# Performance work log

Measured on AMD Instinct MI355X. Metric: run time of the kernel, lower is better.

Reference implementation:

```python
import jax, jax.numpy as jnp
import numpy as np

B, N, D, WIN = 2, 4096, 256, 16


def setup_inputs() -> dict:
    key = jax.random.key(0)
    ks = jax.random.split(key, 10)
    def lin(k, o, i):
        return 0.02 * jax.random.normal(k, (o, i), jnp.float32)
    W = N // WIN
    return {
        "x": 0.5 * jax.random.normal(ks[0], (B, N, D), jnp.float32),
        "embed_qk": jax.random.normal(ks[1], (3, B, W, WIN, WIN, 3), jnp.float32),
        "act_proj_w": lin(ks[2], D, D), "act_proj_b": jnp.zeros((D,), jnp.float32),
        "proj_ln_g": jnp.ones((D,), jnp.float32), "proj_ln_b": jnp.zeros((D,), jnp.float32),
        "conv_w": lin(ks[3], D, D), "conv_b": jnp.zeros((D,), jnp.float32),
        "q_w": lin(ks[4], D, D), "q_b": jnp.zeros((D,), jnp.float32),
        "k_w": lin(ks[5], D, D), "k_b": jnp.zeros((D,), jnp.float32),
        "p_w": lin(ks[6], 1, 3), "p_b": jnp.zeros((1,), jnp.float32),
        "lin_w": lin(ks[7], D, D), "lin_b": jnp.zeros((D,), jnp.float32),
        "norm_g": jnp.ones((D,), jnp.float32), "norm_b": jnp.zeros((D,), jnp.float32),
    }


def _ln(x, g, b, eps=1e-5):
    m = x.mean(-1, keepdims=True)
    v = ((x - m) ** 2).mean(-1, keepdims=True)
    return (x - m) * jax.lax.rsqrt(v + eps) * g + b


def reference(x, embed_qk, act_proj_w, act_proj_b, proj_ln_g, proj_ln_b,
              conv_w, conv_b, q_w, q_b, k_w, k_b, p_w, p_b,
              lin_w, lin_b, norm_g, norm_b):
    # MSMAttentionLayer: gated residual path
    act_res = jax.nn.silu(x @ act_proj_w.T + act_proj_b)          # (B,N,C)
    h = _ln(x, proj_ln_g, proj_ln_b)
    h = jax.nn.silu(h @ conv_w.T + conv_b)                        # 1x1 conv == per-token linear

    # MSMLMultiHeadAttention, stage=1 (window 4x4=16); N % 16 == 0 so add_row_num = 0
    q = jax.nn.elu(h @ q_w.T + q_b) + 1.0
    k = jax.nn.elu(h @ k_w.T + k_b) + 1.0
    v = h
    Bn, Nn, C = h.shape
    Wn = Nn // WIN
    q_win = q.reshape(Bn, Wn, WIN, C)
    k_win = k.reshape(Bn, Wn, WIN, C)
    v_win = v.reshape(Bn, Wn, WIN, C)
    # learned relative-position bias: Linear(3,1) on embed_qk[stage]
    p = (embed_qk[1] @ p_w.T + p_b)[..., 0]
    # second elu+1 feature map (applied on top of q/k which are already elu+1)
    phi_q = jax.nn.elu(q_win) + 1.0
    phi_k = jax.nn.elu(k_win) + 1.0
    # linear-attention style KV aggregation: reduces over windows w
    KV = jnp.einsum('bwmc,bwmd->bmcd', phi_k, v_win)
    att = jnp.einsum('bwnc,bmcd->bwnmd', phi_q, KV) + p[..., None]
    attn_out = att.reshape(Bn, -1, C)[:, :Nn, :]                  # (B,N,C)

    hid = (attn_out * act_res) @ lin_w.T + lin_b
    return _ln(hid + h, norm_g, norm_b)
```

## Files before the change

kernel.cpp:

```cpp
#include <hip/hip_runtime.h>


#define DIM 256
#define NTOK 4096

typedef __attribute__((ext_vector_type(8))) short short8;
typedef __attribute__((ext_vector_type(4))) short short4v;
typedef __attribute__((ext_vector_type(4))) float f32x4;

__device__ __forceinline__ float silu_f(float z) { return z / (1.f + __expf(-z)); }
__device__ __forceinline__ float elu2_f(float z) { return z > 0.f ? z + 2.f : __expf(z) + 1.f; }

__device__ __forceinline__ short f2bf(float f) {
    union { float f; unsigned u; } v; v.f = f;
    unsigned r = v.u + 0x7fffu + ((v.u >> 16) & 1u);
    return (short)(r >> 16);
}
__device__ __forceinline__ float bf2f(short s) {
    union { unsigned u; float f; } v; v.u = ((unsigned)(unsigned short)s) << 16;
    return v.f;
}
__device__ __forceinline__ short8 cvt8(const float* src) {
    const float4 a = *(const float4*)src;
    const float4 c = *(const float4*)(src + 4);
    short8 s;
    s[0] = f2bf(a.x); s[1] = f2bf(a.y); s[2] = f2bf(a.z); s[3] = f2bf(a.w);
    s[4] = f2bf(c.x); s[5] = f2bf(c.y); s[6] = f2bf(c.z); s[7] = f2bf(c.w);
    return s;
}

__global__ __launch_bounds__(256) void fused_dual(
        const float* __restrict__ XF,
        const float* __restrict__ W0f, const float* __restrict__ b0, short* __restrict__ Y0,
        const float* __restrict__ W1f, const float* __restrict__ b1, short* __restrict__ Y1,
        const float* __restrict__ G, const float* __restrict__ Bt) {
    __shared__ __align__(16) short Xs[64 * 72];
    __shared__ __align__(16) short Ws[64 * 72];
    __shared__ float stats[64][2];
    const int zz = blockIdx.z;
    const float* Wf = zz ? W1f : W0f;
    const float* bias = zz ? b1 : b0;
    short* Y = zz ? Y1 : Y0;
    const int tid = threadIdx.x;
    const int wv = tid >> 6, l = tid & 63;
    const int lr = l & 15, lk = l >> 4;
    const int r0 = blockIdx.x * 64, c0 = blockIdx.y * 64;
    const int wm = (wv >> 1) * 32, wn = (wv & 1) * 32;
    const int sr = tid >> 3, sc = (tid & 7) * 8;

    if (zz) {
        const int prow = tid >> 2, pseg = tid & 3;
        const float* src = XF + (size_t)(r0 + prow) * DIM + pseg * 64;
        float a1 = 0.f, a2 = 0.f;
        #pragma unroll
        for (int j = 0; j < 16; ++j) {
            const float4 v = *(const float4*)(src + j * 4);
            a1 += v.x + v.y + v.z + v.w;
            a2 += v.x * v.x + v.y * v.y + v.z * v.z + v.w * v.w;
        }
        a1 += __shfl_xor(a1, 1); a2 += __shfl_xor(a2, 1);
        a1 += __shfl_xor(a1, 2); a2 += __shfl_xor(a2, 2);
        if (pseg == 0) {
            const float mm = a1 * (1.f / DIM);
            stats[prow][0] = mm;
            stats[prow][1] = rsqrtf(a2 * (1.f / DIM) - mm * mm + 1e-5f);
        }
        __syncthreads();
    }

    f32x4 acc[2][2];
    #pragma unroll
    for (int i = 0; i < 2; ++i)
        #pragma unroll
        for (int j = 0; j < 2; ++j) acc[i][j] = (f32x4){0.f, 0.f, 0.f, 0.f};
    for (int kt = 0; kt < DIM; kt += 64) {
        #pragma unroll
        for (int p = 0; p < 2; ++p) {
            const int row = sr + p * 32;
            const float* src = XF + (size_t)(r0 + row) * DIM + kt + sc;
            const float4 a = *(const float4*)src;
            const float4 c = *(const float4*)(src + 4);
            float v[8] = {a.x, a.y, a.z, a.w, c.x, c.y, c.z, c.w};
            short8 s;
            if (zz) {
                const float mm = stats[row][0], rs = stats[row][1];
                const float4 g1 = *(const float4*)(G + kt + sc);
                const float4 g2 = *(const float4*)(G + kt + sc + 4);
                const float4 t1 = *(const float4*)(Bt + kt + sc);
                const float4 t2 = *(const float4*)(Bt + kt + sc + 4);
                const float gv[8] = {g1.x, g1.y, g1.z, g1.w, g2.x, g2.y, g2.z, g2.w};
                const float bv[8] = {t1.x, t1.y, t1.z, t1.w, t2.x, t2.y, t2.z, t2.w};
                #pragma unroll
                for (int j = 0; j < 8; ++j) s[j] = f2bf((v[j] - mm) * rs * gv[j] + bv[j]);
            } else {
                #pragma unroll
                for (int j = 0; j < 8; ++j) s[j] = f2bf(v[j]);
            }
            *(short8*)&Xs[row * 72 + sc] = s;
        }
        #pragma unroll
        for (int p = 0; p < 2; ++p) {
            const int row = sr + p * 32;
            *(short8*)&Ws[row * 72 + sc] = cvt8(Wf + (size_t)(c0 + row) * DIM + kt + sc);
        }
        __syncthreads();
        #pragma unroll
        for (int kc = 0; kc < 2; ++kc) {
            short8 af[2], bfr[2];
            #pragma unroll
            for (int mi = 0; mi < 2; ++mi)
                af[mi] = *(const short8*)&Xs[(wm + mi * 16 + lr) * 72 + kc * 32 + lk * 8];
            #pragma unroll
            for (int ni = 0; ni < 2; ++ni)
                bfr[ni] = *(const short8*)&Ws[(wn + ni * 16 + lr) * 72 + kc * 32 + lk * 8];
            #pragma unroll
            for (int mi = 0; mi < 2; ++mi)
                #pragma unroll
                for (int ni = 0; ni < 2; ++ni)
                    acc[mi][ni] = __builtin_amdgcn_mfma_f32_16x16x32_bf16(af[mi], bfr[ni], acc[mi][ni], 0, 0, 0);
        }
        __syncthreads();
    }
    #pragma unroll
    for (int mi = 0; mi < 2; ++mi)
        #pragma unroll
        for (int ni = 0; ni < 2; ++ni) {
            const int c = c0 + wn + ni * 16 + lr;
            const float bv = bias[c];
            #pragma unroll
            for (int i = 0; i < 4; ++i) {
                const int r = r0 + wm + mi * 16 + lk * 4 + i;
                Y[(size_t)r * DIM + c] = f2bf(silu_f(acc[mi][ni][i] + bv));
            }
        }
}

__global__ __launch_bounds__(256) void gemm_kq(
        const short* __restrict__ H, const float* __restrict__ Wkf, const float* __restrict__ bk, short* __restrict__ PK,
        const float* __restrict__ Wqf, const float* __restrict__ bq, short* __restrict__ PQ) {
    __shared__ __align__(16) short Xs[64 * 72];
    __shared__ __align__(16) short Ws[64 * 72];
    const int bx = blockIdx.x;
    const bool isq = bx >= 128;
    const float* Wf = isq ? Wqf : Wkf;
    const float* bias = isq ? bq : bk;
    short* Y = isq ? PQ : PK;
    const int r0 = (isq ? bx - 128 : bx) * 64;
    const int c0 = blockIdx.y * 64;
    const int tid = threadIdx.x;
    const int wv = tid >> 6, l = tid & 63;
    const int lr = l & 15, lk = l >> 4;
    const int wm = (wv >> 1) * 32, wn = (wv & 1) * 32;
    const int sr = tid >> 3, sc = (tid & 7) * 8;
    f32x4 acc[2][2];
    #pragma unroll
    for (int i = 0; i < 2; ++i)
        #pragma unroll
        for (int j = 0; j < 2; ++j) acc[i][j] = (f32x4){0.f, 0.f, 0.f, 0.f};
    for (int kt = 0; kt < DIM; kt += 64) {
        #pragma unroll
        for (int p = 0; p < 2; ++p) {
            const int row = sr + p * 32;
            int grow = r0 + row;
            if (isq) grow = ((grow >> 8) << 12) + (grow & 255);
            *(short8*)&Xs[row * 72 + sc] = *(const short8*)(H + (size_t)grow * DIM + kt + sc);
        }
        #pragma unroll
        for (int p = 0; p < 2; ++p) {
            const int row = sr + p * 32;
            *(short8*)&Ws[row * 72 + sc] = cvt8(Wf + (size_t)(c0 + row) * DIM + kt + sc);
        }
        __syncthreads();
        #pragma unroll
        for (int kc = 0; kc < 2; ++kc) {
            short8 af[2], bfr[2];
            #pragma unroll
            for (int mi = 0; mi < 2; ++mi)
                af[mi] = *(const short8*)&Xs[(wm + mi * 16 + lr) * 72 + kc * 32 + lk * 8];
            #pragma unroll
            for (int ni = 0; ni < 2; ++ni)
                bfr[ni] = *(const short8*)&Ws[(wn + ni * 16 + lr) * 72 + kc * 32 + lk * 8];
            #pragma unroll
            for (int mi = 0; mi < 2; ++mi)
                #pragma unroll
                for (int ni = 0; ni < 2; ++ni)
                    acc[mi][ni] = __builtin_amdgcn_mfma_f32_16x16x32_bf16(af[mi], bfr[ni], acc[mi][ni], 0, 0, 0);
        }
        __syncthreads();
    }
    #pragma unroll
    for (int mi = 0; mi < 2; ++mi)
        #pragma unroll
        for (int ni = 0; ni < 2; ++ni) {
            const int c = c0 + wn + ni * 16 + lr;
            const float bv = bias[c];
            #pragma unroll
            for (int i = 0; i < 4; ++i) {
                const int r = r0 + wm + mi * 16 + lk * 4 + i;
                Y[(size_t)r * DIM + c] = f2bf(elu2_f(acc[mi][ni][i] + bv));
            }
        }
}

__global__ __launch_bounds__(256) void kv_mfma(const short* __restrict__ HB, const short* __restrict__ PK,
                                               short* __restrict__ KVT) {
    __shared__ __align__(16) short Hs[64 * 68];
    __shared__ __align__(16) short Ps[64 * 68];
    const int tid = threadIdx.x;
    const int bm = blockIdx.x, b = bm >> 4, m = bm & 15;
    const int d0 = blockIdx.y * 64, c0 = blockIdx.z * 64;
    const int wv = tid >> 6, l = tid & 63;
    const int lr = l & 15, lk = l >> 4;
    const int wd = (wv >> 1) * 32, wc = (wv & 1) * 32;
    f32x4 acc[2][2];
    #pragma unroll
    for (int i = 0; i < 2; ++i)
        #pragma unroll
        for (int j = 0; j < 2; ++j) acc[i][j] = (f32x4){0.f, 0.f, 0.f, 0.f};
    const size_t hbase = (size_t)b * NTOK * DIM;
    const int sr = tid >> 3, sc = (tid & 7) * 8;
    for (int kt = 0; kt < 256; kt += 64) {
        #pragma unroll
        for (int p = 0; p < 2; ++p) {
            const int w = sr + p * 32;
            const size_t gg = hbase + (size_t)((kt + w) * 16 + m) * DIM;
            short8 hv = *(const short8*)(HB + gg + d0 + sc);
            short8 pv = *(const short8*)(PK + gg + c0 + sc);
            *(short4v*)&Hs[w * 68 + sc]     = __builtin_shufflevector(hv, hv, 0, 1, 2, 3);
            *(short4v*)&Hs[w * 68 + sc + 4] = __builtin_shufflevector(hv, hv, 4, 5, 6, 7);
            *(short4v*)&Ps[w * 68 + sc]     = __builtin_shufflevector(pv, pv, 0, 1, 2, 3);
            *(short4v*)&Ps[w * 68 + sc + 4] = __builtin_shufflevector(pv, pv, 4, 5, 6, 7);
        }
        __syncthreads();
        #pragma unroll
        for (int kc = 0; kc < 2; ++kc) {
            const int kb = kc * 32 + lk * 8;
            short8 af[2], bfr[2];
            #pragma unroll
            for (int di = 0; di < 2; ++di)
                #pragma unroll
                for (int i = 0; i < 8; ++i)
                    af[di][i] = Hs[(kb + i) * 68 + wd + di * 16 + lr];
            #pragma unroll
            for (int ci = 0; ci < 2; ++ci)
                #pragma unroll
                for (int i = 0; i < 8; ++i)
                    bfr[ci][i] = Ps[(kb + i) * 68 + wc + ci * 16 + lr];
            #pragma unroll
            for (int di = 0; di < 2; ++di)
                #pragma unroll
                for (int ci = 0; ci < 2; ++ci)
                    acc[di][ci] = __builtin_amdgcn_mfma_f32_16x16x32_bf16(af[di], bfr[ci], acc[di][ci], 0, 0, 0);
        }
        __syncthreads();
    }
    #pragma unroll
    for (int di = 0; di < 2; ++di)
        #pragma unroll
        for (int ci = 0; ci < 2; ++ci)
            #pragma unroll
            for (int i = 0; i < 4; ++i) {
                const int d = d0 + wd + di * 16 + lk * 4 + i;
                const int c = c0 + wc + ci * 16 + lr;
                KVT[((size_t)bm * DIM + d) * DIM + c] = f2bf(acc[di][ci][i]);
            }
}

__global__ __launch_bounds__(256) void attlin(
        const short* __restrict__ PQ, const short* __restrict__ KVT,
        const float* __restrict__ emb, const float* __restrict__ pw, const float* __restrict__ pb,
        const short* __restrict__ AR,
        const float* __restrict__ WLf, const float* __restrict__ bl,
        const short* __restrict__ HB, const float* __restrict__ G, const float* __restrict__ Bt,
        float* __restrict__ Y) {
    __shared__ __align__(16) short Qs[32 * 264];
    __shared__ __align__(16) short AGs[32 * 264];
    __shared__ __align__(16) short Bs[256 * 72];
    __shared__ float s1buf[32][2];
    __shared__ float s2buf[32][2];
    const int tid = threadIdx.x;
    const int wv = tid >> 6, l = tid & 63;
    const int lr = l & 15, lk = l >> 4;
    const int bm = blockIdx.x, b = bm >> 4, m = bm & 15;
    const int q0 = blockIdx.y * 32;
    const int wq = (wv >> 1) * 16;
    const int wd = (wv & 1) * 32;
    const int sr = tid >> 3, sc = (tid & 7) * 8;

    #pragma unroll
    for (int p = 0; p < 4; ++p) {
        const int chunk = tid + p * 256;
        const int row = chunk >> 5, cc = (chunk & 31) * 8;
        *(short8*)&Qs[row * 264 + cc] = *(const short8*)(PQ + (size_t)(b * 256 + q0 + row) * DIM + cc);
    }

    f32x4 accA[4][2];
    #pragma unroll
    for (int i = 0; i < 4; ++i)
        #pragma unroll
        for (int j = 0; j < 2; ++j) accA[i][j] = (f32x4){0.f, 0.f, 0.f, 0.f};
    for (int kt = 0; kt < DIM; kt += 64) {
        #pragma unroll
        for (int p = 0; p < 8; ++p) {
            const int row = sr + p * 32;
            *(short8*)&Bs[row * 72 + sc] = *(const short8*)(KVT + ((size_t)bm * DIM + row) * DIM + kt + sc);
        }
        __syncthreads();
        #pragma unroll
        for (int kc = 0; kc < 2; ++kc) {
            const short8 af = *(const short8*)&Qs[(wq + lr) * 264 + kt + kc * 32 + lk * 8];
            #pragma unroll
            for (int dc = 0; dc < 4; ++dc)
                #pragma unroll
                for (int ni = 0; ni < 2; ++ni) {
                    const short8 bfr = *(const short8*)&Bs[(dc * 64 + wd + ni * 16 + lr) * 72 + kc * 32 + lk * 8];
                    accA[dc][ni] = __builtin_amdgcn_mfma_f32_16x16x32_bf16(af, bfr, accA[dc][ni], 0, 0, 0);
                }
        }
        __syncthreads();
    }
    {
        const float pw0 = pw[0], pw1 = pw[1], pw2 = pw[2], pbv = pb[0];
        #pragma unroll
        for (int i = 0; i < 4; ++i) {
            const int rloc = wq + lk * 4 + i;
            const int qr = q0 + rloc;
            const int widx = qr >> 4, nidx = qr & 15;
            const float* e = emb + ((((size_t)(2 + b) * 256 + widx) * 16 + nidx) * 16 + m) * 3;
            const float pv = e[0] * pw0 + e[1] * pw1 + e[2] * pw2 + pbv;
            const int t = qr * 16 + m;
            #pragma unroll
            for (int dc = 0; dc < 4; ++dc)
                #pragma unroll
                for (int ni = 0; ni < 2; ++ni) {
                    const int d = dc * 64 + wd + ni * 16 + lr;
                    const size_t o = ((size_t)b * NTOK + t) * DIM + d;
                    AGs[rloc * 264 + d] = f2bf((accA[dc][ni][i] + pv) * bf2f(AR[o]));
                }
        }
    }
    __syncthreads();

    const int wn2 = (wv & 1) * 128;
    f32x4 accB[8];
    #pragma unroll
    for (int i = 0; i < 8; ++i) accB[i] = (f32x4){0.f, 0.f, 0.f, 0.f};
    for (int kt = 0; kt < DIM; kt += 64) {
        #pragma unroll
        for (int p = 0; p < 8; ++p) {
            const int row = sr + p * 32;
            *(short8*)&Bs[row * 72 + sc] = cvt8(WLf + (size_t)row * DIM + kt + sc);
        }
        __syncthreads();
        #pragma unroll
        for (int kc = 0; kc < 2; ++kc) {
            const short8 af = *(const short8*)&AGs[(wq + lr) * 264 + kt + kc * 32 + lk * 8];
            #pragma unroll
            for (int ni = 0; ni < 8; ++ni) {
                const short8 bfr = *(const short8*)&Bs[(wn2 + ni * 16 + lr) * 72 + kc * 32 + lk * 8];
                accB[ni] = __builtin_amdgcn_mfma_f32_16x16x32_bf16(af, bfr, accB[ni], 0, 0, 0);
            }
        }
        __syncthreads();
    }
    float s1[4] = {0.f, 0.f, 0.f, 0.f}, s2[4] = {0.f, 0.f, 0.f, 0.f};
    #pragma unroll
    for (int ni = 0; ni < 8; ++ni) {
        const int col = wn2 + ni * 16 + lr;
        const float bv = bl[col];
        #pragma unroll
        for (int i = 0; i < 4; ++i) {
            const int rloc = wq + lk * 4 + i;
            const int t = (q0 + rloc) * 16 + m;
            const float z = accB[ni][i] + bv + bf2f(HB[((size_t)b * NTOK + t) * DIM + col]);
            accB[ni][i] = z;
            s1[i] += z; s2[i] += z * z;
        }
    }
    #pragma unroll
    for (int o = 1; o < 16; o <<= 1) {
        #pragma unroll
        for (int i = 0; i < 4; ++i) {
            s1[i] += __shfl_xor(s1[i], o);
            s2[i] += __shfl_xor(s2[i], o);
        }
    }
    if (lr == 0) {
        #pragma unroll
        for (int i = 0; i < 4; ++i) {
            const int rloc = wq + lk * 4 + i;
            s1buf[rloc][wv & 1] = s1[i];
            s2buf[rloc][wv & 1] = s2[i];
        }
    }
    __syncthreads();
    float mean[4], rstd[4];
    #pragma unroll
    for (int i = 0; i < 4; ++i) {
        const int rloc = wq + lk * 4 + i;
        const float t1 = s1buf[rloc][0] + s1buf[rloc][1];
        const float t2 = s2buf[rloc][0] + s2buf[rloc][1];
        const float mm = t1 * (1.f / DIM);
        mean[i] = mm;
        rstd[i] = rsqrtf(t2 * (1.f / DIM) - mm * mm + 1e-5f);
    }
    #pragma unroll
    for (int ni = 0; ni < 8; ++ni) {
        const int col = wn2 + ni * 16 + lr;
        const float gv = G[col], bv2 = Bt[col];
        #pragma unroll
        for (int i = 0; i < 4; ++i) {
            const int rloc = wq + lk * 4 + i;
            const int t = (q0 + rloc) * 16 + m;
            Y[((size_t)b * NTOK + t) * DIM + col] = (accB[ni][i] - mean[i]) * rstd[i] * gv + bv2;
        }
    }
}

extern "C" void kernel_launch(void* const* d_in, const int* in_sizes, int n_in,
                              void* d_out, int out_size, void* d_ws, size_t ws_size,
                              hipStream_t stream) {
    const float* x   = (const float*)d_in[0];
    const float* emb = (const float*)d_in[1];
    const float* Wa  = (const float*)d_in[2];
    const float* ba  = (const float*)d_in[3];
    const float* lng = (const float*)d_in[4];
    const float* lnb = (const float*)d_in[5];
    const float* Wc  = (const float*)d_in[6];
    const float* bc  = (const float*)d_in[7];
    const float* Wq  = (const float*)d_in[8];
    const float* bq  = (const float*)d_in[9];
    const float* Wk  = (const float*)d_in[10];
    const float* bk  = (const float*)d_in[11];
    const float* pw  = (const float*)d_in[12];
    const float* pb  = (const float*)d_in[13];
    const float* Wl  = (const float*)d_in[14];
    const float* bl  = (const float*)d_in[15];
    const float* ng  = (const float*)d_in[16];
    const float* nb  = (const float*)d_in[17];

    char* ws = (char*)d_ws;
    const size_t MB = 1024 * 1024;
    short* h_bf   = (short*)(ws + 0 * MB);
    short* phik   = (short*)(ws + 4 * MB);
    short* phiq   = (short*)(ws + 8 * MB);
    short* kvT    = (short*)(ws + 9 * MB);
    short* act_bf = (short*)(ws + 13 * MB);

    fused_dual<<<dim3(128, 4, 2), dim3(256), 0, stream>>>(x, Wa, ba, act_bf,
                                                          Wc, bc, h_bf, lng, lnb);
    gemm_kq<<<dim3(136, 4), dim3(256), 0, stream>>>(h_bf, Wk, bk, phik, Wq, bq, phiq);
    kv_mfma<<<dim3(32, 4, 4), dim3(256), 0, stream>>>(h_bf, phik, kvT);
    attlin<<<dim3(32, 8), dim3(256), 0, stream>>>(phiq, kvT, emb, pw, pb, act_bf, Wl, bl,
                                                  h_bf, ng, nb, (float*)d_out);
}
```

Measured before the change: 59.14 us.

## Keep weight slab resident in LDS and loop over multiple row tiles

Both projection GEMM kernels now load a full 64x256 bf16 weight slab into shared memory once per block and reuse it across several 64-row tiles, instead of reconverting fp32 weights every k-step for each tile. Grids shrink (64x4x2 and 66x4), with each block handling 2 row tiles, or 4 for the Q path. This removes redundant global weight loads and fp32-to-bf16 conversion, at the cost of larger LDS use (about 33KB per block) and fewer blocks, which may reduce occupancy and parallelism on a many-CU GPU.

```diff
diff --git a/kernel.cpp b/kernel.cpp
--- a/kernel.cpp
+++ b/kernel.cpp
@@ -29,177 +29,195 @@
     return s;
 }
 
-__global__ __launch_bounds__(256) void fused_dual(
+__global__ __launch_bounds__(256) void gemm_wres_a(
         const float* __restrict__ XF,
-        const float* __restrict__ W0f, const float* __restrict__ b0, short* __restrict__ Y0,
-        const float* __restrict__ W1f, const float* __restrict__ b1, short* __restrict__ Y1,
+        const float* __restrict__ Waf, const float* __restrict__ ba, short* __restrict__ ACT,
+        const float* __restrict__ Wcf, const float* __restrict__ bc, short* __restrict__ H,
         const float* __restrict__ G, const float* __restrict__ Bt) {
+    __shared__ __align__(16) short Wres[64 * 264];
     __shared__ __align__(16) short Xs[64 * 72];
-    __shared__ __align__(16) short Ws[64 * 72];
     __shared__ float stats[64][2];
     const int zz = blockIdx.z;
-    const float* Wf = zz ? W1f : W0f;
-    const float* bias = zz ? b1 : b0;
-    short* Y = zz ? Y1 : Y0;
-    const int tid = threadIdx.x;
-    const int wv = tid >> 6, l = tid & 63;
-    const int lr = l & 15, lk = l >> 4;
-    const int r0 = blockIdx.x * 64, c0 = blockIdx.y * 64;
-    const int wm = (wv >> 1) * 32, wn = (wv & 1) * 32;
-    const int sr = tid >> 3, sc = (tid & 7) * 8;
-
-    if (zz) {
-        const int prow = tid >> 2, pseg = tid & 3;
-        const float* src = XF + (size_t)(r0 + prow) * DIM + pseg * 64;
-        float a1 = 0.f, a2 = 0.f;
-        #pragma unroll
-        for (int j = 0; j < 16; ++j) {
-            const float4 v = *(const float4*)(src + j * 4);
-            a1 += v.x + v.y + v.z + v.w;
-            a2 += v.x * v.x + v.y * v.y + v.z * v.z + v.w * v.w;
-        }
-        a1 += __shfl_xor(a1, 1); a2 += __shfl_xor(a2, 1);
-        a1 += __shfl_xor(a1, 2); a2 += __shfl_xor(a2, 2);
-        if (pseg == 0) {
-            const float mm = a1 * (1.f / DIM);
-            stats[prow][0] = mm;
-            stats[prow][1] = rsqrtf(a2 * (1.f / DIM) - mm * mm + 1e-5f);
-        }
-        __syncthreads();
-    }
-
-    f32x4 acc[2][2];
-    #pragma unroll
-    for (int i = 0; i < 2; ++i)
-        #pragma unroll
-        for (int j = 0; j < 2; ++j) acc[i][j] = (f32x4){0.f, 0.f, 0.f, 0.f};
-    for (int kt = 0; kt < DIM; kt += 64) {
-        #pragma unroll
-        for (int p = 0; p < 2; ++p) {
-            const int row = sr + p * 32;
-            const float* src = XF + (size_t)(r0 + row) * DIM + kt + sc;
-            const float4 a = *(const float4*)src;
-            const float4 c = *(const float4*)(src + 4);
-            float v[8] = {a.x, a.y, a.z, a.w, c.x, c.y, c.z, c.w};
-            short8 s;
-            if (zz) {
-                const float mm = stats[row][0], rs = stats[row][1];
-                const float4 g1 = *(const float4*)(G + kt + sc);
-                const float4 g2 = *(const float4*)(G + kt + sc + 4);
-                const float4 t1 = *(const float4*)(Bt + kt + sc);
-                const float4 t2 = *(const float4*)(Bt + kt + sc + 4);
-                const float gv[8] = {g1.x, g1.y, g1.z, g1.w, g2.x, g2.y, g2.z, g2.w};
-                const float bv[8] = {t1.x, t1.y, t1.z, t1.w, t2.x, t2.y, t2.z, t2.w};
-                #pragma unroll
-                for (int j = 0; j < 8; ++j) s[j] = f2bf((v[j] - mm) * rs * gv[j] + bv[j]);
-            } else {
-                #pragma unroll
-                for (int j = 0; j < 8; ++j) s[j] = f2bf(v[j]);
-            }
-            *(short8*)&Xs[row * 72 + sc] = s;
-        }
-        #pragma unroll
-        for (int p = 0; p < 2; ++p) {
-            const int row = sr + p * 32;
-            *(short8*)&Ws[row * 72 + sc] = cvt8(Wf + (size_t)(c0 + row) * DIM + kt + sc);
-        }
-        __syncthreads();
-        #pragma unroll
-        for (int kc = 0; kc < 2; ++kc) {
-            short8 af[2], bfr[2];
-            #pragma unroll
-            for (int mi = 0; mi < 2; ++mi)
-                af[mi] = *(const short8*)&Xs[(wm + mi * 16 + lr) * 72 + kc * 32 + lk * 8];
-            #pragma unroll
-            for (int ni = 0; ni < 2; ++ni)
-                bfr[ni] = *(const short8*)&Ws[(wn + ni * 16 + lr) * 72 + kc * 32 + lk * 8];
-            #pragma unroll
-            for (int mi = 0; mi < 2; ++mi)
-                #pragma unroll
-                for (int ni = 0; ni < 2; ++ni)
-                    acc[mi][ni] = __builtin_amdgcn_mfma_f32_16x16x32_bf16(af[mi], bfr[ni], acc[mi][ni], 0, 0, 0);
-        }
-        __syncthreads();
-    }
-    #pragma unroll
-    for (int mi = 0; mi < 2; ++mi)
-        #pragma unroll
-        for (int ni = 0; ni < 2; ++ni) {
-            const int c = c0 + wn + ni * 16 + lr;
-            const float bv = bias[c];
-            #pragma unroll
-            for (int i = 0; i < 4; ++i) {
-                const int r = r0 + wm + mi * 16 + lk * 4 + i;
-                Y[(size_t)r * DIM + c] = f2bf(silu_f(acc[mi][ni][i] + bv));
-            }
-        }
-}
-
-__global__ __launch_bounds__(256) void gemm_kq(
-        const short* __restrict__ H, const float* __restrict__ Wkf, const float* __restrict__ bk, short* __restrict__ PK,
-        const float* __restrict__ Wqf, const float* __restrict__ bq, short* __restrict__ PQ) {
-    __shared__ __align__(16) short Xs[64 * 72];
-    __shared__ __align__(16) short Ws[64 * 72];
-    const int bx = blockIdx.x;
-    const bool isq = bx >= 128;
-    const float* Wf = isq ? Wqf : Wkf;
-    const float* bias = isq ? bq : bk;
-    short* Y = isq ? PQ : PK;
-    const int r0 = (isq ? bx - 128 : bx) * 64;
     const int c0 = blockIdx.y * 64;
+    const int rg = blockIdx.x;
+    const float* Wf = zz ? Wcf : Waf;
+    const float* bias = zz ? bc : ba;
+    short* Y = zz ? H : ACT;
     const int tid = threadIdx.x;
     const int wv = tid >> 6, l = tid & 63;
     const int lr = l & 15, lk = l >> 4;
     const int wm = (wv >> 1) * 32, wn = (wv & 1) * 32;
     const int sr = tid >> 3, sc = (tid & 7) * 8;
-    f32x4 acc[2][2];
-    #pragma unroll
-    for (int i = 0; i < 2; ++i)
-        #pragma unroll
-        for (int j = 0; j < 2; ++j) acc[i][j] = (f32x4){0.f, 0.f, 0.f, 0.f};
-    for (int kt = 0; kt < DIM; kt += 64) {
-        #pragma unroll
-        for (int p = 0; p < 2; ++p) {
-            const int row = sr + p * 32;
-            int grow = r0 + row;
-            if (isq) grow = ((grow >> 8) << 12) + (grow & 255);
-            *(short8*)&Xs[row * 72 + sc] = *(const short8*)(H + (size_t)grow * DIM + kt + sc);
-        }
-        #pragma unroll
-        for (int p = 0; p < 2; ++p) {
-            const int row = sr + p * 32;
-            *(short8*)&Ws[row * 72 + sc] = cvt8(Wf + (size_t)(c0 + row) * DIM + kt + sc);
-        }
-        __syncthreads();
-        #pragma unroll
-        for (int kc = 0; kc < 2; ++kc) {
-            short8 af[2], bfr[2];
-            #pragma unroll
-            for (int mi = 0; mi < 2; ++mi)
-                af[mi] = *(const short8*)&Xs[(wm + mi * 16 + lr) * 72 + kc * 32 + lk * 8];
-            #pragma unroll
-            for (int ni = 0; ni < 2; ++ni)
-                bfr[ni] = *(const short8*)&Ws[(wn + ni * 16 + lr) * 72 + kc * 32 + lk * 8];
-            #pragma unroll
-            for (int mi = 0; mi < 2; ++mi)
+
+    {
+        const int row = tid >> 2, cseg = (tid & 3) * 64;
+        const float* wsrc = Wf + (size_t)(c0 + row) * DIM + cseg;
+        #pragma unroll
+        for (int j = 0; j < 8; ++j)
+            *(short8*)&Wres[row * 264 + cseg + j * 8] = cvt8(wsrc + j * 8);
+    }
+    __syncthreads();
+
+    for (int rt = 0; rt < 2; ++rt) {
+        const int r0 = (rg * 2 + rt) * 64;
+        __syncthreads();
+        if (zz) {
+            const int prow = tid >> 2, pseg = tid & 3;
+            const float* src = XF + (size_t)(r0 + prow) * DIM + pseg * 64;
+            float a1 = 0.f, a2 = 0.f;
+            #pragma unroll
+            for (int j = 0; j < 16; ++j) {
+                const float4 v = *(const float4*)(src + j * 4);
+                a1 += v.x + v.y + v.z + v.w;
+                a2 += v.x * v.x + v.y * v.y + v.z * v.z + v.w * v.w;
+            }
+            a1 += __shfl_xor(a1, 1); a2 += __shfl_xor(a2, 1);
+            a1 += __shfl_xor(a1, 2); a2 += __shfl_xor(a2, 2);
+            if (pseg == 0) {
+                const float mm = a1 * (1.f / DIM);
+                stats[prow][0] = mm;
+                stats[prow][1] = rsqrtf(a2 * (1.f / DIM) - mm * mm + 1e-5f);
+            }
+            __syncthreads();
+        }
+        f32x4 acc[2][2];
+        #pragma unroll
+        for (int i = 0; i < 2; ++i)
+            #pragma unroll
+            for (int j = 0; j < 2; ++j) acc[i][j] = (f32x4){0.f, 0.f, 0.f, 0.f};
+        for (int kt = 0; kt < DIM; kt += 64) {
+            #pragma unroll
+            for (int p = 0; p < 2; ++p) {
+                const int row = sr + p * 32;
+                const float* src = XF + (size_t)(r0 + row) * DIM + kt + sc;
+                const float4 a = *(const float4*)src;
+                const float4 c = *(const float4*)(src + 4);
+                float v[8] = {a.x, a.y, a.z, a.w, c.x, c.y, c.z, c.w};
+                short8 s;
+                if (zz) {
+                    const float mm = stats[row][0], rs = stats[row][1];
+                    const float4 g1 = *(const float4*)(G + kt + sc);
+                    const float4 g2 = *(const float4*)(G + kt + sc + 4);
+                    const float4 t1 = *(const float4*)(Bt + kt + sc);
+                    const float4 t2 = *(const float4*)(Bt + kt + sc + 4);
+                    const float gv[8] = {g1.x, g1.y, g1.z, g1.w, g2.x, g2.y, g2.z, g2.w};
+                    const float bv[8] = {t1.x, t1.y, t1.z, t1.w, t2.x, t2.y, t2.z, t2.w};
+                    #pragma unroll
+                    for (int j = 0; j < 8; ++j) s[j] = f2bf((v[j] - mm) * rs * gv[j] + bv[j]);
+                } else {
+                    #pragma unroll
+                    for (int j = 0; j < 8; ++j) s[j] = f2bf(v[j]);
+                }
+                *(short8*)&Xs[row * 72 + sc] = s;
+            }
+            __syncthreads();
+            #pragma unroll
+            for (int kc = 0; kc < 2; ++kc) {
+                short8 af[2], bfr[2];
+                #pragma unroll
+                for (int mi = 0; mi < 2; ++mi)
+                    af[mi] = *(const short8*)&Xs[(wm + mi * 16 + lr) * 72 + kc * 32 + lk * 8];
                 #pragma unroll
                 for (int ni = 0; ni < 2; ++ni)
-                    acc[mi][ni] = __builtin_amdgcn_mfma_f32_16x16x32_bf16(af[mi], bfr[ni], acc[mi][ni], 0, 0, 0);
-        }
-        __syncthreads();
-    }
-    #pragma unroll
-    for (int mi = 0; mi < 2; ++mi)
-        #pragma unroll
-        for (int ni = 0; ni < 2; ++ni) {
-            const int c = c0 + wn + ni * 16 + lr;
-            const float bv = bias[c];
-            #pragma unroll
-            for (int i = 0; i < 4; ++i) {
-                const int r = r0 + wm + mi * 16 + lk * 4 + i;
-                Y[(size_t)r * DIM + c] = f2bf(elu2_f(acc[mi][ni][i] + bv));
-            }
-        }
+                    bfr[ni] = *(const short8*)&Wres[(wn + ni * 16 + lr) * 264 + kt + kc * 32 + lk * 8];
+                #pragma unroll
+                for (int mi = 0; mi < 2; ++mi)
+                    #pragma unroll
+                    for (int ni = 0; ni < 2; ++ni)
+                        acc[mi][ni] = __builtin_amdgcn_mfma_f32_16x16x32_bf16(af[mi], bfr[ni], acc[mi][ni], 0, 0, 0);
+            }
+            __syncthreads();
+        }
+        #pragma unroll
+        for (int mi = 0; mi < 2; ++mi)
+            #pragma unroll
+            for (int ni = 0; ni < 2; ++ni) {
+                const int c = c0 + wn + ni * 16 + lr;
+                const float bv = bias[c];
+                #pragma unroll
+                for (int i = 0; i < 4; ++i) {
+                    const int r = r0 + wm + mi * 16 + lk * 4 + i;
+                    Y[(size_t)r * DIM + c] = f2bf(silu_f(acc[mi][ni][i] + bv));
+                }
+            }
+    }
+}
+
+__global__ __launch_bounds__(256) void kq_wres(
+        const short* __restrict__ Hb, const float* __restrict__ Wkf, const float* __restrict__ bk, short* __restrict__ PK,
+        const float* __restrict__ Wqf, const float* __restrict__ bq, short* __restrict__ PQ) {
+    __shared__ __align__(16) short Wres[64 * 264];
+    __shared__ __align__(16) short Xs[64 * 72];
+    const int bx = blockIdx.x;
+    const bool isq = bx >= 64;
+    const int c0 = blockIdx.y * 64;
+    const float* Wf = isq ? Wqf : Wkf;
+    const float* bias = isq ? bq : bk;
+    short* Y = isq ? PQ : PK;
+    const int nrt = isq ? 4 : 2;
+    const int rbase = isq ? (bx - 64) * 4 : bx * 2;
+    const int tid = threadIdx.x;
+    const int wv = tid >> 6, l = tid & 63;
+    const int lr = l & 15, lk = l >> 4;
+    const int wm = (wv >> 1) * 32, wn = (wv & 1) * 32;
+    const int sr = tid >> 3, sc = (tid & 7) * 8;
+
+    {
+        const int row = tid >> 2, cseg = (tid & 3) * 64;
+        const float* wsrc = Wf + (size_t)(c0 + row) * DIM + cseg;
+        #pragma unroll
+        for (int j = 0; j < 8; ++j)
+            *(short8*)&Wres[row * 264 + cseg + j * 8] = cvt8(wsrc + j * 8);
+    }
+    __syncthreads();
+
+    for (int rt = 0; rt < nrt; ++rt) {
+        const int r0 = (rbase + rt) * 64;
+        __syncthreads();
+        f32x4 acc[2][2];
+        #pragma unroll
+        for (int i = 0; i < 2; ++i)
+            #pragma unroll
+            for (int j = 0; j < 2; ++j) acc[i][j] = (f32x4){0.f, 0.f, 0.f, 0.f};
+        for (int kt = 0; kt < DIM; kt += 64) {
+            #pragma unroll
+            for (int p = 0; p < 2; ++p) {
+                const int row = sr + p * 32;
+                int grow = r0 + row;
+                if (isq) grow = ((grow >> 8) << 12) + (grow & 255);
+                *(short8*)&Xs[row * 72 + sc] = *(const short8*)(Hb + (size_t)grow * DIM + kt + sc);
+            }
+            __syncthreads();
+            #pragma unroll
+            for (int kc = 0; kc < 2; ++kc) {
+                short8 af[2], bfr[2];
+                #pragma unroll
+                for (int mi = 0; mi < 2; ++mi)
+                    af[mi] = *(const short8*)&Xs[(wm + mi * 16 + lr) * 72 + kc * 32 + lk * 8];
+                #pragma unroll
+                for (int ni = 0; ni < 2; ++ni)
+                    bfr[ni] = *(const short8*)&Wres[(wn + ni * 16 + lr) * 264 + kt + kc * 32 + lk * 8];
+                #pragma unroll
+                for (int mi = 0; mi < 2; ++mi)
+                    #pragma unroll
+                    for (int ni = 0; ni < 2; ++ni)
+                        acc[mi][ni] = __builtin_amdgcn_mfma_f32_16x16x32_bf16(af[mi], bfr[ni], acc[mi][ni], 0, 0, 0);
+            }
+            __syncthreads();
+        }
+        #pragma unroll
+        for (int mi = 0; mi < 2; ++mi)
+            #pragma unroll
+            for (int ni = 0; ni < 2; ++ni) {
+                const int c = c0 + wn + ni * 16 + lr;
+                const float bv = bias[c];
+                #pragma unroll
+                for (int i = 0; i < 4; ++i) {
+                    const int r = r0 + wm + mi * 16 + lk * 4 + i;
+                    Y[(size_t)r * DIM + c] = f2bf(elu2_f(acc[mi][ni][i] + bv));
+                }
+            }
+    }
 }
 
 __global__ __launch_bounds__(256) void kv_mfma(const short* __restrict__ HB, const short* __restrict__ PK,
@@ -447,9 +465,9 @@
     short* kvT    = (short*)(ws + 9 * MB);
     short* act_bf = (short*)(ws + 13 * MB);
 
-    fused_dual<<<dim3(128, 4, 2), dim3(256), 0, stream>>>(x, Wa, ba, act_bf,
+    gemm_wres_a<<<dim3(64, 4, 2), dim3(256), 0, stream>>>(x, Wa, ba, act_bf,
                                                           Wc, bc, h_bf, lng, lnb);
-    gemm_kq<<<dim3(136, 4), dim3(256), 0, stream>>>(h_bf, Wk, bk, phik, Wq, bq, phiq);
+    kq_wres<<<dim3(66, 4), dim3(256), 0, stream>>>(h_bf, Wk, bk, phik, Wq, bq, phiq);
     kv_mfma<<<dim3(32, 4, 4), dim3(256), 0, stream>>>(h_bf, phik, kvT);
     attlin<<<dim3(32, 8), dim3(256), 0, stream>>>(phiq, kvT, emb, pw, pb, act_bf, Wl, bl,
                                                   h_bf, ng, nb, (float*)d_out);
```

New measurement: 66.53 us. 12.5% more time.

## Precast K/Q/lin weights to bf16 once and load full-K tiles in single pass

Applied to the files above, without the earlier changes.

The first kernel gains extra blocks that convert the K, Q and output-linear weights to bf16 in workspace, so later kernels read bf16 instead of converting fp32 on every tile load. Both small GEMM kernels now stage the whole K=256 extent into shared memory at once (row stride 264) and run eight MFMA steps after a single barrier, which removes the per-K-tile sync loop. The cost is much more LDS per block (about 66KB), which can lower occupancy. The cast blocks also add a little work to the first launch.

```diff
diff --git a/kernel.cpp b/kernel.cpp
--- a/kernel.cpp
+++ b/kernel.cpp
@@ -28,29 +28,49 @@
     s[4] = f2bf(c.x); s[5] = f2bf(c.y); s[6] = f2bf(c.z); s[7] = f2bf(c.w);
     return s;
 }
-
-__global__ __launch_bounds__(256) void fused_dual(
+__device__ __forceinline__ void cast_chunk(const float* __restrict__ src, short* __restrict__ dst,
+                                           int chunk, int tid) {
+    const int base = chunk * 8192 + tid * 32;
+    #pragma unroll
+    for (int j = 0; j < 4; ++j)
+        *(short8*)(dst + base + j * 8) = cvt8(src + base + j * 8);
+}
+
+#define LDW 264
+
+__global__ __launch_bounds__(256) void dual_fk(
         const float* __restrict__ XF,
         const float* __restrict__ W0f, const float* __restrict__ b0, short* __restrict__ Y0,
         const float* __restrict__ W1f, const float* __restrict__ b1, short* __restrict__ Y1,
-        const float* __restrict__ G, const float* __restrict__ Bt) {
-    __shared__ __align__(16) short Xs[64 * 72];
-    __shared__ __align__(16) short Ws[64 * 72];
+        const float* __restrict__ G, const float* __restrict__ Bt,
+        const float* __restrict__ Wkf, short* __restrict__ WKB,
+        const float* __restrict__ Wqf, short* __restrict__ WQB,
+        const float* __restrict__ Wlf, short* __restrict__ WLB) {
+    const int tid = threadIdx.x;
+    if (blockIdx.x >= 128) {
+        if (blockIdx.y == 0 && blockIdx.z == 0) {
+            const int which = blockIdx.x - 128;
+            if (which < 8) cast_chunk(Wkf, WKB, which, tid);
+            else if (which < 16) cast_chunk(Wqf, WQB, which - 8, tid);
+            else cast_chunk(Wlf, WLB, which - 16, tid);
+        }
+        return;
+    }
+    __shared__ __align__(16) short Xs[64 * LDW];
+    __shared__ __align__(16) short Ws[64 * LDW];
     __shared__ float stats[64][2];
     const int zz = blockIdx.z;
     const float* Wf = zz ? W1f : W0f;
     const float* bias = zz ? b1 : b0;
     short* Y = zz ? Y1 : Y0;
-    const int tid = threadIdx.x;
+    const int r0 = blockIdx.x * 64, c0 = blockIdx.y * 64;
     const int wv = tid >> 6, l = tid & 63;
     const int lr = l & 15, lk = l >> 4;
-    const int r0 = blockIdx.x * 64, c0 = blockIdx.y * 64;
     const int wm = (wv >> 1) * 32, wn = (wv & 1) * 32;
-    const int sr = tid >> 3, sc = (tid & 7) * 8;
+    const int srow = tid >> 2, scol = (tid & 3) * 64;
 
     if (zz) {
-        const int prow = tid >> 2, pseg = tid & 3;
-        const float* src = XF + (size_t)(r0 + prow) * DIM + pseg * 64;
+        const float* src = XF + (size_t)(r0 + srow) * DIM + scol;
         float a1 = 0.f, a2 = 0.f;
         #pragma unroll
         for (int j = 0; j < 16; ++j) {
@@ -60,66 +80,67 @@
         }
         a1 += __shfl_xor(a1, 1); a2 += __shfl_xor(a2, 1);
         a1 += __shfl_xor(a1, 2); a2 += __shfl_xor(a2, 2);
-        if (pseg == 0) {
+        if ((tid & 3) == 0) {
             const float mm = a1 * (1.f / DIM);
-            stats[prow][0] = mm;
-            stats[prow][1] = rsqrtf(a2 * (1.f / DIM) - mm * mm + 1e-5f);
-        }
-        __syncthreads();
-    }
-
-    f32x4 acc[2][2];
-    #pragma unroll
-    for (int i = 0; i < 2; ++i)
-        #pragma unroll
-        for (int j = 0; j < 2; ++j) acc[i][j] = (f32x4){0.f, 0.f, 0.f, 0.f};
-    for (int kt = 0; kt < DIM; kt += 64) {
-        #pragma unroll
-        for (int p = 0; p < 2; ++p) {
-            const int row = sr + p * 32;
-            const float* src = XF + (size_t)(r0 + row) * DIM + kt + sc;
+            stats[srow][0] = mm;
+            stats[srow][1] = rsqrtf(a2 * (1.f / DIM) - mm * mm + 1e-5f);
+        }
+        __syncthreads();
+    }
+
+    if (zz) {
+        const float mm = stats[srow][0], rs = stats[srow][1];
+        #pragma unroll
+        for (int j = 0; j < 8; ++j) {
+            const float* src = XF + (size_t)(r0 + srow) * DIM + scol + j * 8;
             const float4 a = *(const float4*)src;
             const float4 c = *(const float4*)(src + 4);
-            float v[8] = {a.x, a.y, a.z, a.w, c.x, c.y, c.z, c.w};
+            const float4 g1 = *(const float4*)(G + scol + j * 8);
+            const float4 g2 = *(const float4*)(G + scol + j * 8 + 4);
+            const float4 t1 = *(const float4*)(Bt + scol + j * 8);
+            const float4 t2 = *(const float4*)(Bt + scol + j * 8 + 4);
             short8 s;
-            if (zz) {
-                const float mm = stats[row][0], rs = stats[row][1];
-                const float4 g1 = *(const float4*)(G + kt + sc);
-                const float4 g2 = *(const float4*)(G + kt + sc + 4);
-                const float4 t1 = *(const float4*)(Bt + kt + sc);
-                const float4 t2 = *(const float4*)(Bt + kt + sc + 4);
-                const float gv[8] = {g1.x, g1.y, g1.z, g1.w, g2.x, g2.y, g2.z, g2.w};
-                const float bv[8] = {t1.x, t1.y, t1.z, t1.w, t2.x, t2.y, t2.z, t2.w};
-                #pragma unroll
-                for (int j = 0; j < 8; ++j) s[j] = f2bf((v[j] - mm) * rs * gv[j] + bv[j]);
-            } else {
-                #pragma unroll
-                for (int j = 0; j < 8; ++j) s[j] = f2bf(v[j]);
-            }
-            *(short8*)&Xs[row * 72 + sc] = s;
-        }
-        #pragma unroll
-        for (int p = 0; p < 2; ++p) {
-            const int row = sr + p * 32;
-            *(short8*)&Ws[row * 72 + sc] = cvt8(Wf + (size_t)(c0 + row) * DIM + kt + sc);
-        }
-        __syncthreads();
-        #pragma unroll
-        for (int kc = 0; kc < 2; ++kc) {
-            short8 af[2], bfr[2];
-            #pragma unroll
-            for (int mi = 0; mi < 2; ++mi)
-                af[mi] = *(const short8*)&Xs[(wm + mi * 16 + lr) * 72 + kc * 32 + lk * 8];
+            s[0] = f2bf((a.x - mm) * rs * g1.x + t1.x);
+            s[1] = f2bf((a.y - mm) * rs * g1.y + t1.y);
+            s[2] = f2bf((a.z - mm) * rs * g1.z + t1.z);
+            s[3] = f2bf((a.w - mm) * rs * g1.w + t1.w);
+            s[4] = f2bf((c.x - mm) * rs * g2.x + t2.x);
+            s[5] = f2bf((c.y - mm) * rs * g2.y + t2.y);
+            s[6] = f2bf((c.z - mm) * rs * g2.z + t2.z);
+            s[7] = f2bf((c.w - mm) * rs * g2.w + t2.w);
+            *(short8*)&Xs[srow * LDW + scol + j * 8] = s;
+        }
+    } else {
+        #pragma unroll
+        for (int j = 0; j < 8; ++j)
+            *(short8*)&Xs[srow * LDW + scol + j * 8] =
+                cvt8(XF + (size_t)(r0 + srow) * DIM + scol + j * 8);
+    }
+    #pragma unroll
+    for (int j = 0; j < 8; ++j)
+        *(short8*)&Ws[srow * LDW + scol + j * 8] =
+            cvt8(Wf + (size_t)(c0 + srow) * DIM + scol + j * 8);
+    __syncthreads();
+
+    f32x4 acc[2][2];
+    #pragma unroll
+    for (int i = 0; i < 2; ++i)
+        #pragma unroll
+        for (int j = 0; j < 2; ++j) acc[i][j] = (f32x4){0.f, 0.f, 0.f, 0.f};
+    #pragma unroll
+    for (int kc = 0; kc < 8; ++kc) {
+        short8 af[2], bfr[2];
+        #pragma unroll
+        for (int mi = 0; mi < 2; ++mi)
+            af[mi] = *(const short8*)&Xs[(wm + mi * 16 + lr) * LDW + kc * 32 + lk * 8];
+        #pragma unroll
+        for (int ni = 0; ni < 2; ++ni)
+            bfr[ni] = *(const short8*)&Ws[(wn + ni * 16 + lr) * LDW + kc * 32 + lk * 8];
+        #pragma unroll
+        for (int mi = 0; mi < 2; ++mi)
             #pragma unroll
             for (int ni = 0; ni < 2; ++ni)
-                bfr[ni] = *(const short8*)&Ws[(wn + ni * 16 + lr) * 72 + kc * 32 + lk * 8];
-            #pragma unroll
-            for (int mi = 0; mi < 2; ++mi)
-                #pragma unroll
-                for (int ni = 0; ni < 2; ++ni)
-                    acc[mi][ni] = __builtin_amdgcn_mfma_f32_16x16x32_bf16(af[mi], bfr[ni], acc[mi][ni], 0, 0, 0);
-        }
-        __syncthreads();
+                acc[mi][ni] = __builtin_amdgcn_mfma_f32_16x16x32_bf16(af[mi], bfr[ni], acc[mi][ni], 0, 0, 0);
     }
     #pragma unroll
     for (int mi = 0; mi < 2; ++mi)
@@ -135,14 +156,14 @@
         }
 }
 
-__global__ __launch_bounds__(256) void gemm_kq(
-        const short* __restrict__ H, const float* __restrict__ Wkf, const float* __restrict__ bk, short* __restrict__ PK,
-        const float* __restrict__ Wqf, const float* __restrict__ bq, short* __restrict__ PQ) {
-    __shared__ __align__(16) short Xs[64 * 72];
-    __shared__ __align__(16) short Ws[64 * 72];
+__global__ __launch_bounds__(256) void kq_fk(
+        const short* __restrict__ H, const short* __restrict__ WKB, const float* __restrict__ bk, short* __restrict__ PK,
+        const short* __restrict__ WQB, const float* __restrict__ bq, short* __restrict__ PQ) {
+    __shared__ __align__(16) short Xs[64 * LDW];
+    __shared__ __align__(16) short Ws[64 * LDW];
     const int bx = blockIdx.x;
     const bool isq = bx >= 128;
-    const float* Wf = isq ? Wqf : Wkf;
+    const short* W = isq ? WQB : WKB;
     const float* bias = isq ? bq : bk;
     short* Y = isq ? PQ : PK;
     const int r0 = (isq ? bx - 128 : bx) * 64;
@@ -151,42 +172,41 @@
     const int wv = tid >> 6, l = tid & 63;
     const int lr = l & 15, lk = l >> 4;
     const int wm = (wv >> 1) * 32, wn = (wv & 1) * 32;
-    const int sr = tid >> 3, sc = (tid & 7) * 8;
+    const int srow = tid >> 2, scol = (tid & 3) * 64;
+
+    {
+        int grow = r0 + srow;
+        if (isq) grow = ((grow >> 8) << 12) + (grow & 255);
+        #pragma unroll
+        for (int j = 0; j < 8; ++j)
+            *(short8*)&Xs[srow * LDW + scol + j * 8] =
+                *(const short8*)(H + (size_t)grow * DIM + scol + j * 8);
+        #pragma unroll
+        for (int j = 0; j < 8; ++j)
+            *(short8*)&Ws[srow * LDW + scol + j * 8] =
+                *(const short8*)(W + (size_t)(c0 + srow) * DIM + scol + j * 8);
+    }
+    __syncthreads();
+
     f32x4 acc[2][2];
     #pragma unroll
     for (int i = 0; i < 2; ++i)
         #pragma unroll
         for (int j = 0; j < 2; ++j) acc[i][j] = (f32x4){0.f, 0.f, 0.f, 0.f};
-    for (int kt = 0; kt < DIM; kt += 64) {
-        #pragma unroll
-        for (int p = 0; p < 2; ++p) {
-            const int row = sr + p * 32;
-            int grow = r0 + row;
-            if (isq) grow = ((grow >> 8) << 12) + (grow & 255);
-            *(short8*)&Xs[row * 72 + sc] = *(const short8*)(H + (size_t)grow * DIM + kt + sc);
-        }
-        #pragma unroll
-        for (int p = 0; p < 2; ++p) {
-            const int row = sr + p * 32;
-            *(short8*)&Ws[row * 72 + sc] = cvt8(Wf + (size_t)(c0 + row) * DIM + kt + sc);
-        }
-        __syncthreads();
-        #pragma unroll
-        for (int kc = 0; kc < 2; ++kc) {
-            short8 af[2], bfr[2];
-            #pragma unroll
-            for (int mi = 0; mi < 2; ++mi)
-                af[mi] = *(const short8*)&Xs[(wm + mi * 16 + lr) * 72 + kc * 32 + lk * 8];
+    #pragma unroll
+    for (int kc = 0; kc < 8; ++kc) {
+        short8 af[2], bfr[2];
+        #pragma unroll
+        for (int mi = 0; mi < 2; ++mi)
+            af[mi] = *(const short8*)&Xs[(wm + mi * 16 + lr) * LDW + kc * 32 + lk * 8];
+        #pragma unroll
+        for (int ni = 0; ni < 2; ++ni)
+            bfr[ni] = *(const short8*)&Ws[(wn + ni * 16 + lr) * LDW + kc * 32 + lk * 8];
+        #pragma unroll
+        for (int mi = 0; mi < 2; ++mi)
             #pragma unroll
             for (int ni = 0; ni < 2; ++ni)
-                bfr[ni] = *(const short8*)&Ws[(wn + ni * 16 + lr) * 72 + kc * 32 + lk * 8];
-            #pragma unroll
-            for (int mi = 0; mi < 2; ++mi)
-                #pragma unroll
-                for (int ni = 0; ni < 2; ++ni)
-                    acc[mi][ni] = __builtin_amdgcn_mfma_f32_16x16x32_bf16(af[mi], bfr[ni], acc[mi][ni], 0, 0, 0);
-        }
-        __syncthreads();
+                acc[mi][ni] = __builtin_amdgcn_mfma_f32_16x16x32_bf16(af[mi], bfr[ni], acc[mi][ni], 0, 0, 0);
     }
     #pragma unroll
     for (int mi = 0; mi < 2; ++mi)
@@ -221,8 +241,8 @@
     const int sr = tid >> 3, sc = (tid & 7) * 8;
     for (int kt = 0; kt < 256; kt += 64) {
         #pragma unroll
-        for (int p = 0; p < 2; ++p) {
-            const int w = sr + p * 32;
+        for (int pp = 0; pp < 2; ++pp) {
+            const int w = sr + pp * 32;
             const size_t gg = hbase + (size_t)((kt + w) * 16 + m) * DIM;
             short8 hv = *(const short8*)(HB + gg + d0 + sc);
             short8 pv = *(const short8*)(PK + gg + c0 + sc);
@@ -270,7 +290,7 @@
         const short* __restrict__ PQ, const short* __restrict__ KVT,
         const float* __restrict__ emb, const float* __restrict__ pw, const float* __restrict__ pb,
         const short* __restrict__ AR,
-        const float* __restrict__ WLf, const float* __restrict__ bl,
+        const short* __restrict__ WLB, const float* __restrict__ bl,
         const short* __restrict__ HB, const float* __restrict__ G, const float* __restrict__ Bt,
         float* __restrict__ Y) {
     __shared__ __align__(16) short Qs[32 * 264];
@@ -288,8 +308,8 @@
     const int sr = tid >> 3, sc = (tid & 7) * 8;
 
     #pragma unroll
-    for (int p = 0; p < 4; ++p) {
-        const int chunk = tid + p * 256;
+    for (int pp = 0; pp < 4; ++pp) {
+        const int chunk = tid + pp * 256;
         const int row = chunk >> 5, cc = (chunk & 31) * 8;
         *(short8*)&Qs[row * 264 + cc] = *(const short8*)(PQ + (size_t)(b * 256 + q0 + row) * DIM + cc);
     }
@@ -301,8 +321,8 @@
         for (int j = 0; j < 2; ++j) accA[i][j] = (f32x4){0.f, 0.f, 0.f, 0.f};
     for (int kt = 0; kt < DIM; kt += 64) {
         #pragma unroll
-        for (int p = 0; p < 8; ++p) {
-            const int row = sr + p * 32;
+        for (int pp = 0; pp < 8; ++pp) {
+            const int row = sr + pp * 32;
             *(short8*)&Bs[row * 72 + sc] = *(const short8*)(KVT + ((size_t)bm * DIM + row) * DIM + kt + sc);
         }
         __syncthreads();
@@ -347,9 +367,9 @@
     for (int i = 0; i < 8; ++i) accB[i] = (f32x4){0.f, 0.f, 0.f, 0.f};
     for (int kt = 0; kt < DIM; kt += 64) {
         #pragma unroll
-        for (int p = 0; p < 8; ++p) {
-            const int row = sr + p * 32;
-            *(short8*)&Bs[row * 72 + sc] = cvt8(WLf + (size_t)row * DIM + kt + sc);
+        for (int pp = 0; pp < 8; ++pp) {
+            const int row = sr + pp * 32;
+            *(short8*)&Bs[row * 72 + sc] = *(const short8*)(WLB + (size_t)row * DIM + kt + sc);
         }
         __syncthreads();
         #pragma unroll
@@ -446,11 +466,15 @@
     short* phiq   = (short*)(ws + 8 * MB);
     short* kvT    = (short*)(ws + 9 * MB);
     short* act_bf = (short*)(ws + 13 * MB);
-
-    fused_dual<<<dim3(128, 4, 2), dim3(256), 0, stream>>>(x, Wa, ba, act_bf,
-                                                          Wc, bc, h_bf, lng, lnb);
-    gemm_kq<<<dim3(136, 4), dim3(256), 0, stream>>>(h_bf, Wk, bk, phik, Wq, bq, phiq);
+    short* Wk_bf  = (short*)(ws + 17 * MB);
+    short* Wq_bf  = (short*)(ws + 17 * MB + 128 * 1024);
+    short* Wl_bf  = (short*)(ws + 17 * MB + 256 * 1024);
+
+    dual_fk<<<dim3(152, 4, 2), dim3(256), 0, stream>>>(x, Wa, ba, act_bf,
+                                                       Wc, bc, h_bf, lng, lnb,
+                                                       Wk, Wk_bf, Wq, Wq_bf, Wl, Wl_bf);
+    kq_fk<<<dim3(136, 4), dim3(256), 0, stream>>>(h_bf, Wk_bf, bk, phik, Wq_bf, bq, phiq);
     kv_mfma<<<dim3(32, 4, 4), dim3(256), 0, stream>>>(h_bf, phik, kvT);
-    attlin<<<dim3(32, 8), dim3(256), 0, stream>>>(phiq, kvT, emb, pw, pb, act_bf, Wl, bl,
+    attlin<<<dim3(32, 8), dim3(256), 0, stream>>>(phiq, kvT, emb, pw, pb, act_bf, Wl_bf, bl,
                                                   h_bf, ng, nb, (float*)d_out);
 }
```

After: 66.07 us. +11.7%, slower.
